# Optimization experiments

Measured on AMD Instinct MI355X. Metric: run time of the kernel, lower is better.

## Reference

```python
import jax, jax.numpy as jnp
import numpy as np

N = 50000
E = 800000
NODE_IN = 64
EDGE_IN = 8
OUT = 1
SAGE_DIMS = [(64, 64), (64, 64), (64, 32), (32, 32)]
EDGE_DIMS = [(8, 64), (64, 64), (64, 32), (32, 32)]


def setup_inputs():
    key = jax.random.key(0)
    keys = iter(jax.random.split(key, 64))
    d = {}
    d["x"] = jax.random.normal(next(keys), (N, NODE_IN), jnp.float32)
    d["dis"] = jax.random.normal(next(keys), (E, EDGE_IN), jnp.float32)
    d["edge_index"] = jax.random.randint(next(keys), (2, E), 0, N, dtype=jnp.int32)
    for i, (fi, fo) in enumerate(SAGE_DIMS):
        d[f"s{i}_wl"] = jax.random.normal(next(keys), (fi, fo), jnp.float32) / np.sqrt(fi).astype(np.float32)
        d[f"s{i}_bl"] = jnp.zeros((fo,), jnp.float32)
        d[f"s{i}_wr"] = jax.random.normal(next(keys), (fi, fo), jnp.float32) / np.sqrt(fi).astype(np.float32)
    for i, (fi, h) in enumerate(EDGE_DIMS):
        d[f"e{i}_w1"] = jax.random.normal(next(keys), (fi, 2 * h), jnp.float32) / np.sqrt(fi).astype(np.float32)
        d[f"e{i}_b1"] = jnp.zeros((2 * h,), jnp.float32)
        d[f"e{i}_w2"] = jax.random.normal(next(keys), (2 * h, h), jnp.float32) / np.sqrt(2 * h).astype(np.float32)
        d[f"e{i}_b2"] = jnp.zeros((h,), jnp.float32)
    d["fc_w"] = jax.random.normal(next(keys), (64, OUT), jnp.float32) / 8.0
    d["fc_b"] = jnp.zeros((OUT,), jnp.float32)
    return d


def _sage(x, row, col, wl, bl, wr):
    # PyG SAGEConv (aggr='mean'): lin_l(mean_{j->i} x_j) + lin_r(x_i); lin_l has bias.
    msg = x[row]  # [E, F] gather of source features
    s = jax.ops.segment_sum(msg, col, num_segments=N)
    cnt = jax.ops.segment_sum(jnp.ones((row.shape[0], 1), x.dtype), col, num_segments=N)
    mean = s / jnp.maximum(cnt, 1.0)  # isolated nodes -> 0 (matches scatter-mean)
    return mean @ wl + bl + x @ wr


def _edge_conv(dis, col, w1, b1, w2, b2):
    # EdgeOnlyConv: add_self_loops with num_nodes=E and zero edge_attr, so the
    # output has E rows; self-loop message = lin(0) = b1 and each segment t gets
    # mean = (sum_{edges->t} lin(dis) + b1) / (deg_in(t) + 1); then lin_update.
    msg = dis @ w1 + b1  # [E, 2h]
    s = jax.ops.segment_sum(msg, col, num_segments=E)
    deg = jax.ops.segment_sum(jnp.ones((col.shape[0], 1), dis.dtype), col, num_segments=E)
    aggr = (s + b1) / (deg + 1.0)
    return aggr @ w2 + b2


def _forward(x, dis, edge_index, sage_params, edge_params, fc_w, fc_b):
    row, col = edge_index[0], edge_index[1]
    h = x
    for wl, bl, wr in sage_params:
        h = jax.nn.leaky_relu(_sage(h, row, col, wl, bl, wr))
    d = dis
    for w1, b1, w2, b2 in edge_params:
        d = jax.nn.leaky_relu(_edge_conv(d, col, w1, b1, w2, b2))
    # dropout is identity at inference
    feats = jnp.concatenate([h[row] * h[col], d], axis=1)  # [E, hidden]
    return feats @ fc_w + fc_b


def reference(x, dis, edge_index, s0_wl, s0_bl, s0_wr, s1_wl, s1_bl, s1_wr, s2_wl, s2_bl, s2_wr, s3_wl, s3_bl, s3_wr, e0_w1, e0_b1, e0_w2, e0_b2, e1_w1, e1_b1, e1_w2, e1_b2, e2_w1, e2_b1, e2_w2, e2_b2, e3_w1, e3_b1, e3_w2, e3_b2, fc_w, fc_b):
    sage_params = [(s0_wl, s0_bl, s0_wr), (s1_wl, s1_bl, s1_wr), (s2_wl, s2_bl, s2_wr), (s3_wl, s3_bl, s3_wr)]
    edge_params = [(e0_w1, e0_b1, e0_w2, e0_b2), (e1_w1, e1_b1, e1_w2, e1_b2), (e2_w1, e2_b1, e2_w2, e2_b2), (e3_w1, e3_b1, e3_w2, e3_b2)]
    return _forward(x, dis, edge_index, sage_params, edge_params, fc_w, fc_b)
```

## Files before the change

kernel.cpp:

```cpp
#include <hip/hip_runtime.h>

#define LRELU(v) ((v) > 0.0f ? (v) : 0.01f * (v))

__device__ __forceinline__ unsigned short f2bf(float f) {
    union { float f; unsigned u; } c;
    c.f = f;
    return (unsigned short)((c.u + 0x7fffu + ((c.u >> 16) & 1)) >> 16);
}
__device__ __forceinline__ float bf_lo(unsigned u) {
    union { unsigned i; float f; } v;
    v.i = u << 16;
    return v.f;
}
__device__ __forceinline__ float bf_hi(unsigned u) {
    union { unsigned i; float f; } v;
    v.i = u & 0xffff0000u;
    return v.f;
}

template <int H2, int HOUT>
__device__ __forceinline__ void w12_body(const float* __restrict__ w1,
                                         const float* __restrict__ w2, float* __restrict__ out,
                                         int i, int o) {
    float s = 0.0f;
// ... 103 lines not shown
            float raw = ps[640 + oo] + ps[672 + oo] + ps[704 + oo] + ps[736 + oo];
            cbuf[448 + oo] = raw;
            float c = LRELU(raw + b2_3[oo]);
            c4s[oo] = c;
            cbuf[160 + oo] = c;
        }
        __syncthreads();
        a = 0.0f;
        if (w < 8) {
            int oo = t & 127, g = t >> 7;
#pragma unroll
            for (int j = 0; j < 16; ++j) {
                int f = g * 16 + j;
                a += c1[f] * w1_1[f * 128 + oo];
            }
        } else if (w < 12) {
            int l = t - 512;
            int oo = l & 63, g = l >> 6;
#pragma unroll
            for (int j = 0; j < 16; ++j) {
                int f = g * 16 + j;
                a += c2[f] * w1_2[f * 64 + oo];
            }
        } else {
            int l = t - 768;
            int oo = l & 63, g = l >> 6;
#pragma unroll
            for (int j = 0; j < 8; ++j) {
                int f = g * 8 + j;
                a += c3[f] * w1_3[f * 64 + oo];
            }
        }
        ps[t] = a;
        __syncthreads();
        if (t < 128) {
            u1[t] = ps[t] + ps[t + 128] + ps[t + 256] + ps[t + 384];
        } else if (t < 192) {
            int oo = t - 128;
            u2[oo] = ps[512 + oo] + ps[576 + oo] + ps[640 + oo] + ps[704 + oo];
        } else if (t < 256) {
            int oo = t - 192;
            u3[oo] = ps[768 + oo] + ps[832 + oo] + ps[896 + oo] + ps[960 + oo];
        }
        __syncthreads();
        a = 0.0f;
        if (w < 4) {
            int oo = t & 63, g = t >> 6;
#pragma unroll
            for (int j = 0; j < 32; ++j) {
                int k = g * 32 + j;
                a += u1[k] * w2_1[k * 64 + oo];
            }
        } else if (w < 6) {
            int l = t - 256;
            int oo = l & 31, g = l >> 5;
#pragma unroll
            for (int j = 0; j < 16; ++j) {
                int k = g * 16 + j;
                a += u2[k] * w2_2[k * 32 + oo];
            }
        } else if (w < 8) {
            int l = t - 384;
            int oo = l & 31, g = l >> 5;
#pragma unroll
            for (int j = 0; j < 16; ++j) {
                int k = g * 16 + j;
                a += u3[k] * w2_3[k * 32 + oo];
            }
        }
        ps[t] = a;
        if (w == 8) {
            int l = t - 512;
            float v = (l < 32) ? c4s[l] * fcw[32 + l] : 0.0f;
            v += __shfl_down(v, 16);
            v += __shfl_down(v, 8);
            v += __shfl_down(v, 4);
            v += __shfl_down(v, 2);
            v += __shfl_down(v, 1);
            if (l == 0) cbuf[512] = v;
        }
        __syncthreads();
        if (t < 64) {
            cbuf[320 + t] = cbuf[256 + t] + ps[t] + ps[t + 64] + ps[t + 128] + ps[t + 192];
        } else if (t < 96) {
            int oo = t - 64;
            cbuf[416 + oo] = cbuf[384 + oo] + ps[256 + oo] + ps[288 + oo] + ps[320 + oo] +
                             ps[352 + oo];
        } else if (t < 128) {
            int oo = t - 96;
            cbuf[480 + oo] = cbuf[448 + oo] + ps[384 + oo] + ps[416 + oo] + ps[448 + oo] +
                             ps[480 + oo];
        }
    }
}

__global__ void bucket_scan_k(const int* __restrict__ bpart, int* __restrict__ bbase,
                              int* __restrict__ bwp, int NBUCK, int E, int EB) {
    __shared__ int s[512];
    int tid = threadIdx.x;
    int v = 0;
    if (tid < NBUCK) {
        for (int b = 0; b < EB; ++b) v += bpart[(size_t)b * 512 + tid];
    }
    s[tid] = v;
    __syncthreads();
    for (int off = 1; off < 512; off <<= 1) {
        int t = (tid >= off) ? s[tid - off] : 0;
        __syncthreads();
        s[tid] += t;
        __syncthreads();
    }
    if (tid < NBUCK) {
        int ex = s[tid] - v;
        bbase[tid] = ex;
        bwp[tid] = ex;
    }
    if (tid == 0) bbase[NBUCK] = E;
}

__global__ void bucket_scatter_k(const int* __restrict__ row, const int* __restrict__ col,
                                 int* __restrict__ bwp, int2* __restrict__ tmp, int E) {
    __shared__ int lcnt[512];
    __shared__ int gbase[512];
    int tid = threadIdx.x;
    for (int i = tid; i < 512; i += 1024) lcnt[i] = 0;
    __syncthreads();
    int base = blockIdx.x * 8192;
    int lpos[8], bk[8];
    for (int k = 0; k < 8; ++k) {
        int e = base + k * 1024 + tid;
        if (e < E) {
            int b = col[e] >> 7;
            bk[k] = b;
            lpos[k] = atomicAdd(&lcnt[b], 1);
        } else
            bk[k] = -1;
    }
    __syncthreads();
    for (int i = tid; i < 512; i += 1024) {
        int v = lcnt[i];
        gbase[i] = v ? atomicAdd(&bwp[i], v) : 0;
    }
    __syncthreads();
    for (int k = 0; k < 8; ++k) {
        int e = base + k * 1024 + tid;
        if (e < E) {
            int c = col[e];
            tmp[gbase[bk[k]] + lpos[k]] = make_int2(row[e], ((c & 127) << 25) | e);
        }
    }
}

template <int FIN, int FOUT>
__device__ __forceinline__ void gemm2_body(const float* __restrict__ h,
                                           const float* __restrict__ wl,
                                           const float* __restrict__ wr,
                                           const float* __restrict__ bl,
                                           unsigned short* __restrict__ hl,
                                           float* __restrict__ hr, int N, int bx, int tid,
                                           float* sw) {
    constexpr int XT = (2 * FOUT) / 4;
    constexpr int NPT = 4;
    constexpr int NPB = (256 / XT) * NPT;
    int tx = tid % XT, ty = tid / XT;
    for (int idx = tid; idx < FIN * FOUT; idx += 256) {
        int f = idx / FOUT, o = idx % FOUT;
        sw[f * 2 * FOUT + o] = wl[idx];
        sw[f * 2 * FOUT + FOUT + o] = wr[idx];
    }
    __syncthreads();
    int og = tx * 4;
    int base = bx * NPB + ty * NPT;
    int ix[NPT] = {min(base + 0, N - 1), min(base + 1, N - 1), min(base + 2, N - 1),
                   min(base + 3, N - 1)};
    float4 s[NPT] = {{0.f, 0.f, 0.f, 0.f}, {0.f, 0.f, 0.f, 0.f}, {0.f, 0.f, 0.f, 0.f},
                     {0.f, 0.f, 0.f, 0.f}};
#pragma unroll 2
    for (int f = 0; f < FIN; f += 4) {
        float4 w0 = *(const float4*)&sw[(f + 0) * 2 * FOUT + og];
        float4 w1 = *(const float4*)&sw[(f + 1) * 2 * FOUT + og];
        float4 w2 = *(const float4*)&sw[(f + 2) * 2 * FOUT + og];
        float4 w3 = *(const float4*)&sw[(f + 3) * 2 * FOUT + og];
#pragma unroll
        for (int k = 0; k < NPT; ++k) {
            float4 v = *(const float4*)(h + (size_t)ix[k] * FIN + f);
            s[k].x += v.x * w0.x + v.y * w1.x + v.z * w2.x + v.w * w3.x;
            s[k].y += v.x * w0.y + v.y * w1.y + v.z * w2.y + v.w * w3.y;
            s[k].z += v.x * w0.z + v.y * w1.z + v.z * w2.z + v.w * w3.z;
            s[k].w += v.x * w0.w + v.y * w1.w + v.z * w2.w + v.w * w3.w;
        }
    }
    bool isR = og >= FOUT;
    int oo = isR ? og - FOUT : og;
    if (isR) {
        float4 bias = *(const float4*)&bl[oo];
#pragma unroll
        for (int k = 0; k < NPT; ++k) {
            int i = base + k;
            if (i < N) {
                float4 r = {s[k].x + bias.x, s[k].y + bias.y, s[k].z + bias.z, s[k].w + bias.w};
                *(float4*)(hr + (size_t)i * FOUT + oo) = r;
            }
        }
    } else {
#pragma unroll
        for (int k = 0; k < NPT; ++k) {
            int i = base + k;
            if (i < N) {
                unsigned short* d = hl + (size_t)i * FOUT + oo;
                *(ushort4*)d = make_ushort4(f2bf(s[k].x), f2bf(s[k].y), f2bf(s[k].z), f2bf(s[k].w));
            }
        }
    }
}

#define RED8(off)                                                                   \
    a0 += __shfl_down(a0, off); a1 += __shfl_down(a1, off);                         \
    a2 += __shfl_down(a2, off); a3 += __shfl_down(a3, off);                         \
    a4 += __shfl_down(a4, off); a5 += __shfl_down(a5, off);                         \
    a6 += __shfl_down(a6, off); a7 += __shfl_down(a7, off);

__device__ __forceinline__ void aggr64_body(const unsigned short* __restrict__ hlb,
                                            const float* __restrict__ hr,
                                            const int* __restrict__ rowptr,
                                            const int* __restrict__ rows,
                                            float* __restrict__ out, int N, int wave, int lane) {
    if (wave >= N) return;
    int u = lane >> 3, f8 = lane & 7;
    int s = rowptr[wave], e = rowptr[wave + 1];
    int l8 = lane & 7;
    const float4* hp = (const float4*)(hr + (size_t)wave * 64) + l8 * 2;
    float4 r0h = hp[0], r1h = hp[1];
    float inv = 1.0f / fmaxf((float)(e - s), 1.0f);
    float a0 = 0.f, a1 = 0.f, a2 = 0.f, a3 = 0.f, a4 = 0.f, a5 = 0.f, a6 = 0.f, a7 = 0.f;
    int p = s + u;
    for (; p + 8 < e; p += 16) {
        int r0 = rows[p], r1 = rows[p + 8];
        uint4 v0 = ((const uint4*)(hlb + (size_t)r0 * 64))[f8];
        uint4 v1 = ((const uint4*)(hlb + (size_t)r1 * 64))[f8];
        a0 += bf_lo(v0.x) + bf_lo(v1.x); a1 += bf_hi(v0.x) + bf_hi(v1.x);
        a2 += bf_lo(v0.y) + bf_lo(v1.y); a3 += bf_hi(v0.y) + bf_hi(v1.y);
        a4 += bf_lo(v0.z) + bf_lo(v1.z); a5 += bf_hi(v0.z) + bf_hi(v1.z);
        a6 += bf_lo(v0.w) + bf_lo(v1.w); a7 += bf_hi(v0.w) + bf_hi(v1.w);
    }
    if (p < e) {
        uint4 v = ((const uint4*)(hlb + (size_t)rows[p] * 64))[f8];
        a0 += bf_lo(v.x); a1 += bf_hi(v.x); a2 += bf_lo(v.y); a3 += bf_hi(v.y);
        a4 += bf_lo(v.z); a5 += bf_hi(v.z); a6 += bf_lo(v.w); a7 += bf_hi(v.w);
    }
    RED8(32) RED8(16) RED8(8)
    if (lane < 8) {
        float4 o0, o1;
        o0.x = LRELU(a0 * inv + r0h.x); o0.y = LRELU(a1 * inv + r0h.y);
        o0.z = LRELU(a2 * inv + r0h.z); o0.w = LRELU(a3 * inv + r0h.w);
        o1.x = LRELU(a4 * inv + r1h.x); o1.y = LRELU(a5 * inv + r1h.y);
        o1.z = LRELU(a6 * inv + r1h.z); o1.w = LRELU(a7 * inv + r1h.w);
        float4* op = (float4*)(out + (size_t)wave * 64) + lane * 2;
        op[0] = o0;
        op[1] = o1;
    }
}

template <bool OUTBF>
__device__ __forceinline__ void aggr32_body(const unsigned short* __restrict__ hlb,
                                            const float* __restrict__ hr,
                                            const int* __restrict__ rowptr,
                                            const int* __restrict__ rows, void* __restrict__ out,
                                            int N, int wave, int lane) {
    if (wave >= N) return;
    int u = lane >> 2, f8 = lane & 3;
    int s = rowptr[wave], e = rowptr[wave + 1];
    int l4 = lane & 3;
    const float4* hp = (const float4*)(hr + (size_t)wave * 32) + l4 * 2;
    float4 r0h = hp[0], r1h = hp[1];
    float inv = 1.0f / fmaxf((float)(e - s), 1.0f);
    float a0 = 0.f, a1 = 0.f, a2 = 0.f, a3 = 0.f, a4 = 0.f, a5 = 0.f, a6 = 0.f, a7 = 0.f;
    int p = s + u;
    for (; p + 16 < e; p += 32) {
        int r0 = rows[p], r1 = rows[p + 16];
        uint4 v0 = ((const uint4*)(hlb + (size_t)r0 * 32))[f8];
        uint4 v1 = ((const uint4*)(hlb + (size_t)r1 * 32))[f8];
        a0 += bf_lo(v0.x) + bf_lo(v1.x); a1 += bf_hi(v0.x) + bf_hi(v1.x);
        a2 += bf_lo(v0.y) + bf_lo(v1.y); a3 += bf_hi(v0.y) + bf_hi(v1.y);
        a4 += bf_lo(v0.z) + bf_lo(v1.z); a5 += bf_hi(v0.z) + bf_hi(v1.z);
        a6 += bf_lo(v0.w) + bf_lo(v1.w); a7 += bf_hi(v0.w) + bf_hi(v1.w);
    }
    if (p < e) {
        uint4 v = ((const uint4*)(hlb + (size_t)rows[p] * 32))[f8];
        a0 += bf_lo(v.x); a1 += bf_hi(v.x); a2 += bf_lo(v.y); a3 += bf_hi(v.y);
        a4 += bf_lo(v.z); a5 += bf_hi(v.z); a6 += bf_lo(v.w); a7 += bf_hi(v.w);
    }
    RED8(32) RED8(16) RED8(8) RED8(4)
    if (lane < 4) {
        float o0 = LRELU(a0 * inv + r0h.x), o1 = LRELU(a1 * inv + r0h.y);
        float o2 = LRELU(a2 * inv + r0h.z), o3 = LRELU(a3 * inv + r0h.w);
        float o4 = LRELU(a4 * inv + r1h.x), o5 = LRELU(a5 * inv + r1h.y);
        float o6 = LRELU(a6 * inv + r1h.z), o7 = LRELU(a7 * inv + r1h.w);
        if (OUTBF) {
            unsigned short* d = (unsigned short*)out + (size_t)wave * 32 + lane * 8;
            *(ushort4*)d = make_ushort4(f2bf(o0), f2bf(o1), f2bf(o2), f2bf(o3));
            *(ushort4*)(d + 4) = make_ushort4(f2bf(o4), f2bf(o5), f2bf(o6), f2bf(o7));
        } else {
            float4* op = (float4*)((float*)out + (size_t)wave * 32) + lane * 2;
            op[0] = make_float4(o0, o1, o2, o3);
            op[1] = make_float4(o4, o5, o6, o7);
        }
    }
}

__device__ __forceinline__ void edge_aggr8_body(const float* __restrict__ dis,
                                                const int* __restrict__ rowptr,
                                                const int* __restrict__ eids,
                                                float* __restrict__ sd, float* __restrict__ zbuf,
                                                int N, int wave, int lane) {
    if (wave >= N) return;
    zbuf[(size_t)wave * 64 + lane] = 0.0f;
    int u = lane >> 1, f4 = lane & 1;
    int s = rowptr[wave], e = rowptr[wave + 1];
    float4 a = {0.f, 0.f, 0.f, 0.f};
    for (int p = s + u; p < e; p += 32) {
        const float4* dp = (const float4*)(dis + (size_t)eids[p] * 8);
        float4 v = dp[f4];
        a.x += v.x; a.y += v.y; a.z += v.z; a.w += v.w;
    }
    for (int off = 32; off >= 2; off >>= 1) {
        a.x += __shfl_down(a.x, off); a.y += __shfl_down(a.y, off);
        a.z += __shfl_down(a.z, off); a.w += __shfl_down(a.w, off);
    }
    if (lane < 2) ((float4*)(sd + (size_t)wave * 8))[f4] = a;
}

template <int FIN, int FOUT>
__device__ __forceinline__ void esc_body(const float* __restrict__ sd, const int* __restrict__ cnt,
                                         const float* __restrict__ w12,
                                         const float* __restrict__ mw2,
                                         const float* __restrict__ b1w2,
                                         const float* __restrict__ b2,
                                         const float* __restrict__ cnext,
                                         const int* __restrict__ col, float* __restrict__ sdnext,
                                         int N, float* __restrict__ zbuf, int zf4, int bx,
                                         int nblk, int tid, float* sw) {
    constexpr int NPT = 4;
    constexpr int NPB = (256 / FOUT) * NPT;
    int o = tid % FOUT, ty = tid / FOUT;
    for (int idx = tid; idx < FIN * FOUT; idx += 256) sw[idx] = w12[idx];
    __syncthreads();
    if (zf4) {
        float4 z4 = {0.f, 0.f, 0.f, 0.f};
        for (int z = bx * 256 + tid; z < zf4; z += nblk * 256) ((float4*)zbuf)[z] = z4;
    }
    int base = bx * NPB + ty * NPT;
    int ix[NPT] = {min(base + 0, N - 1), min(base + 1, N - 1), min(base + 2, N - 1),
                   min(base + 3, N - 1)};
    float s[NPT] = {0.f, 0.f, 0.f, 0.f};
#pragma unroll 2
    for (int f = 0; f < FIN; f += 4) {
        float w0 = sw[(f + 0) * FOUT + o], w1 = sw[(f + 1) * FOUT + o];
        float w2 = sw[(f + 2) * FOUT + o], w3 = sw[(f + 3) * FOUT + o];
#pragma unroll
        for (int k = 0; k < NPT; ++k) {
            float4 v = *(const float4*)(sd + (size_t)ix[k] * FIN + f);
            s[k] += v.x * w0 + v.y * w1 + v.z * w2 + v.w * w3;
        }
    }
    float mo = mw2[o], bo = b1w2[o], b2o = b2[o], co = cnext[o];
#pragma unroll
    for (int k = 0; k < NPT; ++k) {
        int i = base + k;
        if (i < N) {
            float deg = (float)cnt[i];
            float inv = 1.0f / (deg + 1.0f);
            float val = LRELU((s[k] + deg * mo + bo) * inv + b2o);
            atomicAdd(&sdnext[(size_t)col[i] * FOUT + o], val - co);
        }
    }
}

__device__ __forceinline__ void edot_body(const float* __restrict__ sd,
                                          const int* __restrict__ cnt,
                                          const float* __restrict__ w12,
                                          const float* __restrict__ mw2,
                                          const float* __restrict__ b1w2,
                                          const float* __restrict__ b2,
                                          const float* __restrict__ fcw, float* __restrict__ ddot,
                                          int N, int bx, int tid, float* sw) {
    constexpr int FIN = 32, FOUT = 32;
    constexpr int NPT = 4;
    constexpr int NPB = (256 / FOUT) * NPT;
    int o = tid % 32, ty = tid / 32;
    for (int idx = tid; idx < FIN * FOUT; idx += 256) sw[idx] = w12[idx];
    __syncthreads();
    int base = bx * NPB + ty * NPT;
    int ix[NPT] = {min(base + 0, N - 1), min(base + 1, N - 1), min(base + 2, N - 1),
                   min(base + 3, N - 1)};
    float s[NPT] = {0.f, 0.f, 0.f, 0.f};
#pragma unroll 2
    for (int f = 0; f < FIN; f += 4) {
        float w0 = sw[(f + 0) * FOUT + o], w1 = sw[(f + 1) * FOUT + o];
        float w2 = sw[(f + 2) * FOUT + o], w3 = sw[(f + 3) * FOUT + o];
#pragma unroll
        for (int k = 0; k < NPT; ++k) {
            float4 v = *(const float4*)(sd + (size_t)ix[k] * FIN + f);
            s[k] += v.x * w0 + v.y * w1 + v.z * w2 + v.w * w3;
        }
    }
    float mo = mw2[o], bo = b1w2[o], b2o = b2[o], fw = fcw[32 + o];
#pragma unroll
    for (int k = 0; k < NPT; ++k) {
        float deg = (float)cnt[ix[k]];
        float inv = 1.0f / (deg + 1.0f);
        float v = LRELU((s[k] + deg * mo + bo) * inv + b2o) * fw;
        v += __shfl_down(v, 16);
        v += __shfl_down(v, 8);
        v += __shfl_down(v, 4);
        v += __shfl_down(v, 2);
        v += __shfl_down(v, 1);
        if (o == 0 && base + k < N) ddot[base + k] = v;
    }
}

union __align__(16) CsrGemmSM {
    struct {
        int2 buf[3072];
        int lcnt[128];
        int sscan[128];
        int lwp[128];
    } c;
    float sw[64 * 128];
};

__global__ void csr_gemm0_k(const int2* __restrict__ tmp, const int* __restrict__ bbase,
                            int* __restrict__ rowptr, int* __restrict__ cnt,
                            int* __restrict__ rows, int* __restrict__ eids, int N, int E,
                            int NBUCK, const float* __restrict__ h, const float* __restrict__ wl,
                            const float* __restrict__ wr, const float* __restrict__ bl,
                            unsigned short* __restrict__ hl, float* __restrict__ hr) {
    __shared__ CsrGemmSM sm;
    int tid = threadIdx.x;
    if (blockIdx.x < NBUCK) {
        constexpr int CAP = 3072;
        int b = blockIdx.x;
        int s = bbase[b], e = bbase[b + 1];
        int sz = e - s;
        if (tid < 128) sm.c.lcnt[tid] = 0;
        __syncthreads();
        for (int i = tid; i < sz; i += 256) {
            int2 v = tmp[s + i];
            if (i < CAP) sm.c.buf[i] = v;
            atomicAdd(&sm.c.lcnt[((unsigned)v.y) >> 25], 1);
        }
        __syncthreads();
        if (tid < 128) sm.c.sscan[tid] = sm.c.lcnt[tid];
        __syncthreads();
        for (int off = 1; off < 128; off <<= 1) {
            int t = (tid < 128 && tid >= off) ? sm.c.sscan[tid - off] : 0;
            __syncthreads();
            if (tid < 128) sm.c.sscan[tid] += t;
            __syncthreads();
        }
        if (tid < 128) {
            int ex = sm.c.sscan[tid] - sm.c.lcnt[tid];
            sm.c.lwp[tid] = ex;
            int c = b * 128 + tid;
            if (c < N) {
                rowptr[c] = s + ex;
                cnt[c] = sm.c.lcnt[tid];
                if (c == N - 1) rowptr[N] = E;
            }
        }
        __syncthreads();
        for (int i = tid; i < sz; i += 256) {
            int2 v = (i < CAP) ? sm.c.buf[i] : tmp[s + i];
            int cl = ((unsigned)v.y) >> 25;
            int p = atomicAdd(&sm.c.lwp[cl], 1);
            rows[s + p] = v.x;
            eids[s + p] = v.y & 0x1FFFFFF;
        }
        return;
    }
    gemm2_body<64, 64>(h, wl, wr, bl, hl, hr, N, blockIdx.x - NBUCK, tid, sm.sw);
}

__global__ void ag64_ea8_k(const unsigned short* __restrict__ hlb, const float* __restrict__ hr,
                           const int* __restrict__ rowptr, const int* __restrict__ rows,
                           float* __restrict__ out, const float* __restrict__ dis,
                           const int* __restrict__ eids, float* __restrict__ sd0,
                           float* __restrict__ zS1, int N, int NB) {
    int lane = threadIdx.x & 63;
    if (blockIdx.x < NB) {
        int wave = (blockIdx.x * 256 + threadIdx.x) >> 6;
        aggr64_body(hlb, hr, rowptr, rows, out, N, wave, lane);
    } else {
        int wave = ((blockIdx.x - NB) * 256 + threadIdx.x) >> 6;
        edge_aggr8_body(dis, rowptr, eids, sd0, zS1, N, wave, lane);
    }
}

__global__ void g64_esc0_k(const float* __restrict__ h, const float* __restrict__ wl,
                           const float* __restrict__ wr, const float* __restrict__ bl,
                           unsigned short* __restrict__ hl, float* __restrict__ hr,
                           const float* __restrict__ sd0, const int* __restrict__ cnt,
                           const float* __restrict__ w12, const float* __restrict__ mw2,
                           const float* __restrict__ b1w2, const float* __restrict__ b2,
                           const float* __restrict__ cnext, const int* __restrict__ col,
                           float* __restrict__ S1, float* __restrict__ zS2, int N, int G0,
                           int E0) {
    __shared__ float sw[64 * 128];
    int tid = threadIdx.x;
    if (blockIdx.x < G0) {
        gemm2_body<64, 64>(h, wl, wr, bl, hl, hr, N, blockIdx.x, tid, sw);
    } else {
        esc_body<8, 64>(sd0, cnt, w12, mw2, b1w2, b2, cnext, col, S1, N, zS2, N * 16,
                        blockIdx.x - G0, E0, tid, sw);
    }
}

__global__ void ag64_esc1_k(const unsigned short* __restrict__ hlb, const float* __restrict__ hr,
                            const int* __restrict__ rowptr, const int* __restrict__ rows,
                            float* __restrict__ out, const float* __restrict__ S1,
                            const int* __restrict__ cnt, const float* __restrict__ w12,
                            const float* __restrict__ mw2, const float* __restrict__ b1w2,
                            const float* __restrict__ b2, const float* __restrict__ cnext,
                            const int* __restrict__ col, float* __restrict__ S2,
                            float* __restrict__ zS3, int N, int NB, int E0) {
    __shared__ float sw[64 * 64];
    int tid = threadIdx.x;
    if (blockIdx.x < NB) {
        int wave = (blockIdx.x * 256 + tid) >> 6;
        aggr64_body(hlb, hr, rowptr, rows, out, N, wave, tid & 63);
    } else {
        esc_body<64, 64>(S1, cnt, w12, mw2, b1w2, b2, cnext, col, S2, N, zS3, N * 8,
                         blockIdx.x - NB, E0, tid, sw);
    }
}

__global__ void g32_esc2_k(const float* __restrict__ h, const float* __restrict__ wl,
                           const float* __restrict__ wr, const float* __restrict__ bl,
                           unsigned short* __restrict__ hl, float* __restrict__ hr,
                           const float* __restrict__ S2, const int* __restrict__ cnt,
                           const float* __restrict__ w12, const float* __restrict__ mw2,
                           const float* __restrict__ b1w2, const float* __restrict__ b2,
                           const float* __restrict__ cnext, const int* __restrict__ col,
                           float* __restrict__ S3, int N, int G2, int E2) {
    __shared__ float sw[64 * 64];
    int tid = threadIdx.x;
    if (blockIdx.x < G2) {
        gemm2_body<64, 32>(h, wl, wr, bl, hl, hr, N, blockIdx.x, tid, sw);
    } else {
        esc_body<64, 32>(S2, cnt, w12, mw2, b1w2, b2, cnext, col, S3, N, nullptr, 0,
                         blockIdx.x - G2, E2, tid, sw);
    }
}

__global__ void ag32_edot_k(const unsigned short* __restrict__ hlb, const float* __restrict__ hr,
                            const int* __restrict__ rowptr, const int* __restrict__ rows,
                            float* __restrict__ out, const float* __restrict__ S3,
                            const int* __restrict__ cnt, const float* __restrict__ w12,
                            const float* __restrict__ mw2, const float* __restrict__ b1w2,
                            const float* __restrict__ b2, const float* __restrict__ fcw,
                            float* __restrict__ ddot, int N, int NB) {
    __shared__ float sw[32 * 32];
    int tid = threadIdx.x;
    if (blockIdx.x < NB) {
        int wave = (blockIdx.x * 256 + tid) >> 6;
        aggr32_body<false>(hlb, hr, rowptr, rows, (void*)out, N, wave, tid & 63);
    } else {
        edot_body(S3, cnt, w12, mw2, b1w2, b2, fcw, ddot, N, blockIdx.x - NB, tid, sw);
    }
}

__global__ void gemm2_32_k(const float* __restrict__ h, const float* __restrict__ wl,
                           const float* __restrict__ wr, const float* __restrict__ bl,
                           unsigned short* __restrict__ hl, float* __restrict__ hr, int N) {
    __shared__ float sw[32 * 64];
    gemm2_body<32, 32>(h, wl, wr, bl, hl, hr, N, blockIdx.x, threadIdx.x, sw);
}

__global__ void ag32bf_k(const unsigned short* __restrict__ hlb, const float* __restrict__ hr,
                         const int* __restrict__ rowptr, const int* __restrict__ rows,
                         unsigned short* __restrict__ h3b, int N) {
    int wave = (blockIdx.x * 256 + threadIdx.x) >> 6;
    aggr32_body<true>(hlb, hr, rowptr, rows, (void*)h3b, N, wave, threadIdx.x & 63);
}

__global__ void final_csr_k(const unsigned short* __restrict__ h3b,
                            const float* __restrict__ ddot, const float* __restrict__ cbuf,
                            const int* __restrict__ rowptr, const int* __restrict__ rows,
                            const int* __restrict__ eids, const float* __restrict__ fcw,
                            const float* __restrict__ fcb, float* __restrict__ out, int N) {
    int wave = (blockIdx.x * blockDim.x + threadIdx.x) >> 6;
    int lane = threadIdx.x & 63;
    if (wave >= N) return;
    int u = lane >> 2, f2 = lane & 3;
    int s = rowptr[wave], e = rowptr[wave + 1];
    uint4 hc = ((const uint4*)(h3b + (size_t)wave * 32))[f2];
    const float4* fw4 = (const float4*)fcw + f2 * 2;
    float4 w0 = fw4[0], w1 = fw4[1];
    float wc0 = bf_lo(hc.x) * w0.x, wc1 = bf_hi(hc.x) * w0.y;
    float wc2 = bf_lo(hc.y) * w0.z, wc3 = bf_hi(hc.y) * w0.w;
    float wc4 = bf_lo(hc.z) * w1.x, wc5 = bf_hi(hc.z) * w1.y;
    float wc6 = bf_lo(hc.w) * w1.z, wc7 = bf_hi(hc.w) * w1.w;
    float fb = fcb[0];
    float cdot = cbuf[512];
    int p = s + u;
    for (; p + 16 < e; p += 32) {
        int ra = rows[p], rb = rows[p + 16];
        int ea_ = eids[p], eb_ = eids[p + 16];
        uint4 va = ((const uint4*)(h3b + (size_t)ra * 32))[f2];
        uint4 vb = ((const uint4*)(h3b + (size_t)rb * 32))[f2];
        float ta = bf_lo(va.x) * wc0 + bf_hi(va.x) * wc1 + bf_lo(va.y) * wc2 +
                   bf_hi(va.y) * wc3 + bf_lo(va.z) * wc4 + bf_hi(va.z) * wc5 +
                   bf_lo(va.w) * wc6 + bf_hi(va.w) * wc7;
        float tb = bf_lo(vb.x) * wc0 + bf_hi(vb.x) * wc1 + bf_lo(vb.y) * wc2 +
                   bf_hi(vb.y) * wc3 + bf_lo(vb.z) * wc4 + bf_hi(vb.z) * wc5 +
                   bf_lo(vb.w) * wc6 + bf_hi(vb.w) * wc7;
        ta += __shfl_down(ta, 2); tb += __shfl_down(tb, 2);
        ta += __shfl_down(ta, 1); tb += __shfl_down(tb, 1);
        if (f2 == 0) {
            out[ea_] = ta + fb + (ea_ < N ? ddot[ea_] : cdot);
            out[eb_] = tb + fb + (eb_ < N ? ddot[eb_] : cdot);
        }
    }
    if (p < e) {
        int ra = rows[p];
        int ea_ = eids[p];
        uint4 va = ((const uint4*)(h3b + (size_t)ra * 32))[f2];
        float ta = bf_lo(va.x) * wc0 + bf_hi(va.x) * wc1 + bf_lo(va.y) * wc2 +
                   bf_hi(va.y) * wc3 + bf_lo(va.z) * wc4 + bf_hi(va.z) * wc5 +
                   bf_lo(va.w) * wc6 + bf_hi(va.w) * wc7;
        ta += __shfl_down(ta, 2);
        ta += __shfl_down(ta, 1);
        if (f2 == 0) out[ea_] = ta + fb + (ea_ < N ? ddot[ea_] : cdot);
    }
}

extern "C" void kernel_launch(void* const* d_in, const int* in_sizes, int n_in, void* d_out,
                              int out_size, void* d_ws, size_t ws_size, hipStream_t stream) {
    const float* x = (const float*)d_in[0];
    const float* dis = (const float*)d_in[1];
    const int* ei = (const int*)d_in[2];
    const float* s_wl[4] = {(const float*)d_in[3], (const float*)d_in[6], (const float*)d_in[9],
                            (const float*)d_in[12]};
    const float* s_bl[4] = {(const float*)d_in[4], (const float*)d_in[7], (const float*)d_in[10],
                            (const float*)d_in[13]};
    const float* s_wr[4] = {(const float*)d_in[5], (const float*)d_in[8], (const float*)d_in[11],
                            (const float*)d_in[14]};
    const float* e_w1[4] = {(const float*)d_in[15], (const float*)d_in[19], (const float*)d_in[23],
                            (const float*)d_in[27]};
    const float* e_b1[4] = {(const float*)d_in[16], (const float*)d_in[20], (const float*)d_in[24],
                            (const float*)d_in[28]};
    const float* e_w2[4] = {(const float*)d_in[17], (const float*)d_in[21], (const float*)d_in[25],
                            (const float*)d_in[29]};
    const float* e_b2[4] = {(const float*)d_in[18], (const float*)d_in[22], (const float*)d_in[26],
                            (const float*)d_in[30]};
    const float* fcw = (const float*)d_in[31];
    const float* fcb = (const float*)d_in[32];

    const int N = in_sizes[0] / 64;
    const int E = in_sizes[1] / 8;
    const int* row = ei;
    const int* col = ei + E;
    const int NBUCK = (N + 127) / 128;
    const int EB = (E + 8191) / 8192;

    auto au = [](size_t v) { return (v + 255) & ~(size_t)255; };
    char* p = (char*)d_ws;
    int* cnt = (int*)p;        p += au((size_t)N * 4);
    int* rowptr = (int*)p;     p += au((size_t)(N + 1) * 4);
    int* bbase = (int*)p;      p += au(513 * 4);
    int* bwp = (int*)p;        p += au(512 * 4);
    float* w12_0 = (float*)p;  p += au(512 * 4);
    float* w12_1 = (float*)p;  p += au(4096 * 4);
    float* w12_2 = (float*)p;  p += au(2048 * 4);
    float* w12_3 = (float*)p;  p += au(1024 * 4);
    float* cbuf = (float*)p;   p += au(544 * 4);
    int* bpart = (int*)p;      p += au((size_t)EB * 512 * 4);
    int* rowsA = (int*)p;      p += au((size_t)E * 4);
    int* eidsA = (int*)p;      p += au((size_t)E * 4);
    unsigned short* T = (unsigned short*)p; p += au((size_t)N * 64 * 2);
    float* R = (float*)p;      p += au((size_t)N * 64 * 4);
    float* H1 = (float*)p;     p += au((size_t)N * 64 * 4);
    float* H2 = (float*)p;     p += au((size_t)N * 64 * 4);
    float* S1 = (float*)p;     p += au((size_t)N * 64 * 4);
    float* S2 = (float*)p;     p += au((size_t)N * 64 * 4);
    float* S3 = (float*)p;     p += au((size_t)N * 32 * 4);
    float* sd0 = (float*)p;    p += au((size_t)N * 8 * 4);
    unsigned short* h3b = (unsigned short*)p; p += au((size_t)N * 32 * 2);
    float* ddot = (float*)p;   p += au((size_t)N * 4);

    int2* tmp = (int2*)S1;

    const int G0 = (N + 31) / 32;
    const int G2 = (N + 63) / 64;
    const int G3 = (N + 63) / 64;
    const int E0 = (N + 15) / 16;
    const int E2 = (N + 31) / 32;
    const int NB = (N + 3) / 4;

    count_w12c_k<<<EB + 169, 1024, 0, stream>>>(
        col, bpart, E, EB, e_w1[0], e_w2[0], w12_0, e_w1[1], e_w2[1], w12_1, e_w1[2], e_w2[2],
        w12_2, e_w1[3], e_w2[3], w12_3, e_b1[0], e_b2[0], e_b1[1], e_b2[1], e_b1[2], e_b2[2],
        e_b1[3], e_b2[3], fcw, cbuf);
    bucket_scan_k<<<1, 512, 0, stream>>>(bpart, bbase, bwp, NBUCK, E, EB);
    bucket_scatter_k<<<EB, 1024, 0, stream>>>(row, col, bwp, tmp, E);
    csr_gemm0_k<<<NBUCK + G0, 256, 0, stream>>>(tmp, bbase, rowptr, cnt, rowsA, eidsA, N, E,
                                                NBUCK, x, s_wl[0], s_wr[0], s_bl[0], T, R);
    ag64_ea8_k<<<2 * NB, 256, 0, stream>>>(T, R, rowptr, rowsA, H1, dis, eidsA, sd0, S1, N, NB);
    g64_esc0_k<<<G0 + E0, 256, 0, stream>>>(H1, s_wl[1], s_wr[1], s_bl[1], T, R, sd0, cnt, w12_0,
                                            cbuf + 192, cbuf + 192, e_b2[0], cbuf + 0, col, S1,
                                            S2, N, G0, E0);
    ag64_esc1_k<<<NB + E0, 256, 0, stream>>>(T, R, rowptr, rowsA, H2, S1, cnt, w12_1, cbuf + 320,
                                             cbuf + 256, e_b2[1], cbuf + 64, col, S2, S3, N, NB,
                                             E0);
    g32_esc2_k<<<G2 + E2, 256, 0, stream>>>(H2, s_wl[2], s_wr[2], s_bl[2], T, R, S2, cnt, w12_2,
                                            cbuf + 416, cbuf + 384, e_b2[2], cbuf + 128, col, S3,
                                            N, G2, E2);
    ag32_edot_k<<<NB + E2, 256, 0, stream>>>(T, R, rowptr, rowsA, H1, S3, cnt, w12_3, cbuf + 480,
                                             cbuf + 448, e_b2[3], fcw, ddot, N, NB);
    gemm2_32_k<<<G3, 256, 0, stream>>>(H1, s_wl[3], s_wr[3], s_bl[3], T, R, N);
    ag32bf_k<<<NB, 256, 0, stream>>>(T, R, rowptr, rowsA, h3b, N);
    final_csr_k<<<NB, 256, 0, stream>>>(h3b, ddot, cbuf, rowptr, rowsA, eidsA, fcw, fcb,
                                        (float*)d_out, N);
}
```

Baseline: 441.2 us.

## Fuse root-weight GEMM and bias into SAGE aggregation kernels, drop R buffer

The GEMM kernels now compute only the neighbour projection h@wl, stored as bf16. The root term h@wr and the bias are computed inside the per-node aggregation wave: each sub-group of lanes handles a slice of input features, and the partial products are folded into the existing shuffle reduction. This removes the fp32 R intermediate and its write and re-read for every layer, and halves the GEMM work and shared memory. In exchange the aggregation kernels read the input features and the wr weights directly from global memory, with extra FLOPs per wave.

```diff
diff --git a/kernel.cpp b/kernel.cpp
--- a/kernel.cpp
+++ b/kernel.cpp
@@ -279,22 +279,15 @@
 }
 
 template <int FIN, int FOUT>
-__device__ __forceinline__ void gemm2_body(const float* __restrict__ h,
+__device__ __forceinline__ void gemmT_body(const float* __restrict__ h,
                                            const float* __restrict__ wl,
-                                           const float* __restrict__ wr,
-                                           const float* __restrict__ bl,
-                                           unsigned short* __restrict__ hl,
-                                           float* __restrict__ hr, int N, int bx, int tid,
-                                           float* sw) {
-    constexpr int XT = (2 * FOUT) / 4;
+                                           unsigned short* __restrict__ hl, int N, int bx,
+                                           int tid, float* sw) {
+    constexpr int XT = FOUT / 4;
     constexpr int NPT = 4;
     constexpr int NPB = (256 / XT) * NPT;
     int tx = tid % XT, ty = tid / XT;
-    for (int idx = tid; idx < FIN * FOUT; idx += 256) {
-        int f = idx / FOUT, o = idx % FOUT;
-        sw[f * 2 * FOUT + o] = wl[idx];
-        sw[f * 2 * FOUT + FOUT + o] = wr[idx];
-    }
+    for (int idx = tid; idx < FIN * FOUT; idx += 256) sw[idx] = wl[idx];
     __syncthreads();
     int og = tx * 4;
     int base = bx * NPB + ty * NPT;
@@ -304,10 +297,10 @@
                      {0.f, 0.f, 0.f, 0.f}};
 #pragma unroll 2
     for (int f = 0; f < FIN; f += 4) {
-        float4 w0 = *(const float4*)&sw[(f + 0) * 2 * FOUT + og];
-        float4 w1 = *(const float4*)&sw[(f + 1) * 2 * FOUT + og];
-        float4 w2 = *(const float4*)&sw[(f + 2) * 2 * FOUT + og];
-        float4 w3 = *(const float4*)&sw[(f + 3) * 2 * FOUT + og];
+        float4 w0 = *(const float4*)&sw[(f + 0) * FOUT + og];
+        float4 w1 = *(const float4*)&sw[(f + 1) * FOUT + og];
+        float4 w2 = *(const float4*)&sw[(f + 2) * FOUT + og];
+        float4 w3 = *(const float4*)&sw[(f + 3) * FOUT + og];
 #pragma unroll
         for (int k = 0; k < NPT; ++k) {
             float4 v = *(const float4*)(h + (size_t)ix[k] * FIN + f);
@@ -317,26 +310,12 @@
             s[k].w += v.x * w0.w + v.y * w1.w + v.z * w2.w + v.w * w3.w;
         }
     }
-    bool isR = og >= FOUT;
-    int oo = isR ? og - FOUT : og;
-    if (isR) {
-        float4 bias = *(const float4*)&bl[oo];
-#pragma unroll
-        for (int k = 0; k < NPT; ++k) {
-            int i = base + k;
-            if (i < N) {
-                float4 r = {s[k].x + bias.x, s[k].y + bias.y, s[k].z + bias.z, s[k].w + bias.w};
-                *(float4*)(hr + (size_t)i * FOUT + oo) = r;
-            }
-        }
-    } else {
-#pragma unroll
-        for (int k = 0; k < NPT; ++k) {
-            int i = base + k;
-            if (i < N) {
-                unsigned short* d = hl + (size_t)i * FOUT + oo;
-                *(ushort4*)d = make_ushort4(f2bf(s[k].x), f2bf(s[k].y), f2bf(s[k].z), f2bf(s[k].w));
-            }
+#pragma unroll
+    for (int k = 0; k < NPT; ++k) {
+        int i = base + k;
+        if (i < N) {
+            unsigned short* d = hl + (size_t)i * FOUT + og;
+            *(ushort4*)d = make_ushort4(f2bf(s[k].x), f2bf(s[k].y), f2bf(s[k].z), f2bf(s[k].w));
         }
     }
 }
@@ -348,23 +327,39 @@
     a6 += __shfl_down(a6, off); a7 += __shfl_down(a7, off);
 
 __device__ __forceinline__ void aggr64_body(const unsigned short* __restrict__ hlb,
-                                            const float* __restrict__ hr,
+                                            const float* __restrict__ h,
+                                            const float* __restrict__ wr,
+                                            const float* __restrict__ bl,
                                             const int* __restrict__ rowptr,
                                             const int* __restrict__ rows,
                                             float* __restrict__ out, int N, int wave, int lane) {
     if (wave >= N) return;
     int u = lane >> 3, f8 = lane & 7;
     int s = rowptr[wave], e = rowptr[wave + 1];
-    int l8 = lane & 7;
-    const float4* hp = (const float4*)(hr + (size_t)wave * 64) + l8 * 2;
-    float4 r0h = hp[0], r1h = hp[1];
+    float r0 = 0.f, r1 = 0.f, r2 = 0.f, r3 = 0.f, r4 = 0.f, r5 = 0.f, r6 = 0.f, r7 = 0.f;
+    {
+        const float4* hp = (const float4*)(h + (size_t)wave * 64 + 8 * u);
+        float4 hA = hp[0], hB = hp[1];
+        float hv0 = hA.x, hv1 = hA.y, hv2 = hA.z, hv3 = hA.w;
+        float hv4 = hB.x, hv5 = hB.y, hv6 = hB.z, hv7 = hB.w;
+        const float* wrb = wr + (size_t)(8 * u) * 64 + 8 * f8;
+#pragma unroll
+        for (int t = 0; t < 8; ++t) {
+            float4 wA = *(const float4*)(wrb + t * 64);
+            float4 wB = *(const float4*)(wrb + t * 64 + 4);
+            float hv = (t == 0) ? hv0 : (t == 1) ? hv1 : (t == 2) ? hv2 : (t == 3) ? hv3
+                       : (t == 4) ? hv4 : (t == 5) ? hv5 : (t == 6) ? hv6 : hv7;
+            r0 += hv * wA.x; r1 += hv * wA.y; r2 += hv * wA.z; r3 += hv * wA.w;
+            r4 += hv * wB.x; r5 += hv * wB.y; r6 += hv * wB.z; r7 += hv * wB.w;
+        }
+    }
     float inv = 1.0f / fmaxf((float)(e - s), 1.0f);
     float a0 = 0.f, a1 = 0.f, a2 = 0.f, a3 = 0.f, a4 = 0.f, a5 = 0.f, a6 = 0.f, a7 = 0.f;
     int p = s + u;
     for (; p + 8 < e; p += 16) {
-        int r0 = rows[p], r1 = rows[p + 8];
-        uint4 v0 = ((const uint4*)(hlb + (size_t)r0 * 64))[f8];
-        uint4 v1 = ((const uint4*)(hlb + (size_t)r1 * 64))[f8];
+        int n0 = rows[p], n1 = rows[p + 8];
+        uint4 v0 = ((const uint4*)(hlb + (size_t)n0 * 64))[f8];
+        uint4 v1 = ((const uint4*)(hlb + (size_t)n1 * 64))[f8];
         a0 += bf_lo(v0.x) + bf_lo(v1.x); a1 += bf_hi(v0.x) + bf_hi(v1.x);
         a2 += bf_lo(v0.y) + bf_lo(v1.y); a3 += bf_hi(v0.y) + bf_hi(v1.y);
         a4 += bf_lo(v0.z) + bf_lo(v1.z); a5 += bf_hi(v0.z) + bf_hi(v1.z);
@@ -375,38 +370,67 @@
         a0 += bf_lo(v.x); a1 += bf_hi(v.x); a2 += bf_lo(v.y); a3 += bf_hi(v.y);
         a4 += bf_lo(v.z); a5 += bf_hi(v.z); a6 += bf_lo(v.w); a7 += bf_hi(v.w);
     }
+    a0 = a0 * inv + r0; a1 = a1 * inv + r1; a2 = a2 * inv + r2; a3 = a3 * inv + r3;
+    a4 = a4 * inv + r4; a5 = a5 * inv + r5; a6 = a6 * inv + r6; a7 = a7 * inv + r7;
     RED8(32) RED8(16) RED8(8)
     if (lane < 8) {
+        const float4* bp = (const float4*)bl + lane * 2;
+        float4 b0 = bp[0], b1 = bp[1];
         float4 o0, o1;
-        o0.x = LRELU(a0 * inv + r0h.x); o0.y = LRELU(a1 * inv + r0h.y);
-        o0.z = LRELU(a2 * inv + r0h.z); o0.w = LRELU(a3 * inv + r0h.w);
-        o1.x = LRELU(a4 * inv + r1h.x); o1.y = LRELU(a5 * inv + r1h.y);
-        o1.z = LRELU(a6 * inv + r1h.z); o1.w = LRELU(a7 * inv + r1h.w);
+        o0.x = LRELU(a0 + b0.x); o0.y = LRELU(a1 + b0.y);
+        o0.z = LRELU(a2 + b0.z); o0.w = LRELU(a3 + b0.w);
+        o1.x = LRELU(a4 + b1.x); o1.y = LRELU(a5 + b1.y);
+        o1.z = LRELU(a6 + b1.z); o1.w = LRELU(a7 + b1.w);
         float4* op = (float4*)(out + (size_t)wave * 64) + lane * 2;
         op[0] = o0;
         op[1] = o1;
     }
 }
 
-template <bool OUTBF>
+template <int FIN, bool OUTBF>
 __device__ __forceinline__ void aggr32_body(const unsigned short* __restrict__ hlb,
-                                            const float* __restrict__ hr,
+                                            const float* __restrict__ h,
+                                            const float* __restrict__ wr,
+                                            const float* __restrict__ bl,
                                             const int* __restrict__ rowptr,
                                             const int* __restrict__ rows, void* __restrict__ out,
                                             int N, int wave, int lane) {
     if (wave >= N) return;
     int u = lane >> 2, f8 = lane & 3;
     int s = rowptr[wave], e = rowptr[wave + 1];
-    int l4 = lane & 3;
-    const float4* hp = (const float4*)(hr + (size_t)wave * 32) + l4 * 2;
-    float4 r0h = hp[0], r1h = hp[1];
+    float r0 = 0.f, r1 = 0.f, r2 = 0.f, r3 = 0.f, r4 = 0.f, r5 = 0.f, r6 = 0.f, r7 = 0.f;
+    if (FIN == 64) {
+        float4 hA = *(const float4*)(h + (size_t)wave * 64 + 4 * u);
+        float hv0 = hA.x, hv1 = hA.y, hv2 = hA.z, hv3 = hA.w;
+        const float* wrb = wr + (size_t)(4 * u) * 32 + 8 * f8;
+#pragma unroll
+        for (int t = 0; t < 4; ++t) {
+            float4 wA = *(const float4*)(wrb + t * 32);
+            float4 wB = *(const float4*)(wrb + t * 32 + 4);
+            float hv = (t == 0) ? hv0 : (t == 1) ? hv1 : (t == 2) ? hv2 : hv3;
+            r0 += hv * wA.x; r1 += hv * wA.y; r2 += hv * wA.z; r3 += hv * wA.w;
+            r4 += hv * wB.x; r5 += hv * wB.y; r6 += hv * wB.z; r7 += hv * wB.w;
+        }
+    } else {
+        float2 hA = *(const float2*)(h + (size_t)wave * 32 + 2 * u);
+        float hv0 = hA.x, hv1 = hA.y;
+        const float* wrb = wr + (size_t)(2 * u) * 32 + 8 * f8;
+#pragma unroll
+        for (int t = 0; t < 2; ++t) {
+            float4 wA = *(const float4*)(wrb + t * 32);
+            float4 wB = *(const float4*)(wrb + t * 32 + 4);
+            float hv = (t == 0) ? hv0 : hv1;
+            r0 += hv * wA.x; r1 += hv * wA.y; r2 += hv * wA.z; r3 += hv * wA.w;
+            r4 += hv * wB.x; r5 += hv * wB.y; r6 += hv * wB.z; r7 += hv * wB.w;
+        }
+    }
     float inv = 1.0f / fmaxf((float)(e - s), 1.0f);
     float a0 = 0.f, a1 = 0.f, a2 = 0.f, a3 = 0.f, a4 = 0.f, a5 = 0.f, a6 = 0.f, a7 = 0.f;
     int p = s + u;
     for (; p + 16 < e; p += 32) {
-        int r0 = rows[p], r1 = rows[p + 16];
-        uint4 v0 = ((const uint4*)(hlb + (size_t)r0 * 32))[f8];
-        uint4 v1 = ((const uint4*)(hlb + (size_t)r1 * 32))[f8];
+        int n0 = rows[p], n1 = rows[p + 16];
+        uint4 v0 = ((const uint4*)(hlb + (size_t)n0 * 32))[f8];
+        uint4 v1 = ((const uint4*)(hlb + (size_t)n1 * 32))[f8];
         a0 += bf_lo(v0.x) + bf_lo(v1.x); a1 += bf_hi(v0.x) + bf_hi(v1.x);
         a2 += bf_lo(v0.y) + bf_lo(v1.y); a3 += bf_hi(v0.y) + bf_hi(v1.y);
         a4 += bf_lo(v0.z) + bf_lo(v1.z); a5 += bf_hi(v0.z) + bf_hi(v1.z);
@@ -417,12 +441,16 @@
         a0 += bf_lo(v.x); a1 += bf_hi(v.x); a2 += bf_lo(v.y); a3 += bf_hi(v.y);
         a4 += bf_lo(v.z); a5 += bf_hi(v.z); a6 += bf_lo(v.w); a7 += bf_hi(v.w);
     }
+    a0 = a0 * inv + r0; a1 = a1 * inv + r1; a2 = a2 * inv + r2; a3 = a3 * inv + r3;
+    a4 = a4 * inv + r4; a5 = a5 * inv + r5; a6 = a6 * inv + r6; a7 = a7 * inv + r7;
     RED8(32) RED8(16) RED8(8) RED8(4)
     if (lane < 4) {
-        float o0 = LRELU(a0 * inv + r0h.x), o1 = LRELU(a1 * inv + r0h.y);
-        float o2 = LRELU(a2 * inv + r0h.z), o3 = LRELU(a3 * inv + r0h.w);
-        float o4 = LRELU(a4 * inv + r1h.x), o5 = LRELU(a5 * inv + r1h.y);
-        float o6 = LRELU(a6 * inv + r1h.z), o7 = LRELU(a7 * inv + r1h.w);
+        const float4* bp = (const float4*)bl + lane * 2;
+        float4 b0 = bp[0], b1 = bp[1];
+        float o0 = LRELU(a0 + b0.x), o1 = LRELU(a1 + b0.y);
+        float o2 = LRELU(a2 + b0.z), o3 = LRELU(a3 + b0.w);
+        float o4 = LRELU(a4 + b1.x), o5 = LRELU(a5 + b1.y);
+        float o6 = LRELU(a6 + b1.z), o7 = LRELU(a7 + b1.w);
         if (OUTBF) {
             unsigned short* d = (unsigned short*)out + (size_t)wave * 32 + lane * 8;
             *(ushort4*)d = make_ushort4(f2bf(o0), f2bf(o1), f2bf(o2), f2bf(o3));
@@ -553,15 +581,14 @@
         int sscan[128];
         int lwp[128];
     } c;
-    float sw[64 * 128];
+    float sw[64 * 64];
 };
 
 __global__ void csr_gemm0_k(const int2* __restrict__ tmp, const int* __restrict__ bbase,
                             int* __restrict__ rowptr, int* __restrict__ cnt,
                             int* __restrict__ rows, int* __restrict__ eids, int N, int E,
                             int NBUCK, const float* __restrict__ h, const float* __restrict__ wl,
-                            const float* __restrict__ wr, const float* __restrict__ bl,
-                            unsigned short* __restrict__ hl, float* __restrict__ hr) {
+                            unsigned short* __restrict__ hl) {
     __shared__ CsrGemmSM sm;
     int tid = threadIdx.x;
     if (blockIdx.x < NBUCK) {
@@ -605,10 +632,11 @@
         }
         return;
     }
-    gemm2_body<64, 64>(h, wl, wr, bl, hl, hr, N, blockIdx.x - NBUCK, tid, sm.sw);
-}
-
-__global__ void ag64_ea8_k(const unsigned short* __restrict__ hlb, const float* __restrict__ hr,
+    gemmT_body<64, 64>(h, wl, hl, N, blockIdx.x - NBUCK, tid, sm.sw);
+}
+
+__global__ void ag64_ea8_k(const unsigned short* __restrict__ hlb, const float* __restrict__ h,
+                           const float* __restrict__ wr, const float* __restrict__ bl,
                            const int* __restrict__ rowptr, const int* __restrict__ rows,
                            float* __restrict__ out, const float* __restrict__ dis,
                            const int* __restrict__ eids, float* __restrict__ sd0,
@@ -616,7 +644,7 @@
     int lane = threadIdx.x & 63;
     if (blockIdx.x < NB) {
         int wave = (blockIdx.x * 256 + threadIdx.x) >> 6;
-        aggr64_body(hlb, hr, rowptr, rows, out, N, wave, lane);
+        aggr64_body(hlb, h, wr, bl, rowptr, rows, out, N, wave, lane);
     } else {
         int wave = ((blockIdx.x - NB) * 256 + threadIdx.x) >> 6;
         edge_aggr8_body(dis, rowptr, eids, sd0, zS1, N, wave, lane);
@@ -624,25 +652,24 @@
 }
 
 __global__ void g64_esc0_k(const float* __restrict__ h, const float* __restrict__ wl,
-                           const float* __restrict__ wr, const float* __restrict__ bl,
-                           unsigned short* __restrict__ hl, float* __restrict__ hr,
-                           const float* __restrict__ sd0, const int* __restrict__ cnt,
-                           const float* __restrict__ w12, const float* __restrict__ mw2,
-                           const float* __restrict__ b1w2, const float* __restrict__ b2,
-                           const float* __restrict__ cnext, const int* __restrict__ col,
-                           float* __restrict__ S1, float* __restrict__ zS2, int N, int G0,
-                           int E0) {
-    __shared__ float sw[64 * 128];
+                           unsigned short* __restrict__ hl, const float* __restrict__ sd0,
+                           const int* __restrict__ cnt, const float* __restrict__ w12,
+                           const float* __restrict__ mw2, const float* __restrict__ b1w2,
+                           const float* __restrict__ b2, const float* __restrict__ cnext,
+                           const int* __restrict__ col, float* __restrict__ S1,
+                           float* __restrict__ zS2, int N, int G0, int E0) {
+    __shared__ float sw[64 * 64];
     int tid = threadIdx.x;
     if (blockIdx.x < G0) {
-        gemm2_body<64, 64>(h, wl, wr, bl, hl, hr, N, blockIdx.x, tid, sw);
+        gemmT_body<64, 64>(h, wl, hl, N, blockIdx.x, tid, sw);
     } else {
         esc_body<8, 64>(sd0, cnt, w12, mw2, b1w2, b2, cnext, col, S1, N, zS2, N * 16,
                         blockIdx.x - G0, E0, tid, sw);
     }
 }
 
-__global__ void ag64_esc1_k(const unsigned short* __restrict__ hlb, const float* __restrict__ hr,
+__global__ void ag64_esc1_k(const unsigned short* __restrict__ hlb, const float* __restrict__ h,
+                            const float* __restrict__ wr, const float* __restrict__ bl,
                             const int* __restrict__ rowptr, const int* __restrict__ rows,
                             float* __restrict__ out, const float* __restrict__ S1,
                             const int* __restrict__ cnt, const float* __restrict__ w12,
@@ -654,7 +681,7 @@
     int tid = threadIdx.x;
     if (blockIdx.x < NB) {
         int wave = (blockIdx.x * 256 + tid) >> 6;
-        aggr64_body(hlb, hr, rowptr, rows, out, N, wave, tid & 63);
+        aggr64_body(hlb, h, wr, bl, rowptr, rows, out, N, wave, tid & 63);
     } else {
         esc_body<64, 64>(S1, cnt, w12, mw2, b1w2, b2, cnext, col, S2, N, zS3, N * 8,
                          blockIdx.x - NB, E0, tid, sw);
@@ -662,24 +689,24 @@
 }
 
 __global__ void g32_esc2_k(const float* __restrict__ h, const float* __restrict__ wl,
-                           const float* __restrict__ wr, const float* __restrict__ bl,
-                           unsigned short* __restrict__ hl, float* __restrict__ hr,
-                           const float* __restrict__ S2, const int* __restrict__ cnt,
-                           const float* __restrict__ w12, const float* __restrict__ mw2,
-                           const float* __restrict__ b1w2, const float* __restrict__ b2,
-                           const float* __restrict__ cnext, const int* __restrict__ col,
-                           float* __restrict__ S3, int N, int G2, int E2) {
-    __shared__ float sw[64 * 64];
+                           unsigned short* __restrict__ hl, const float* __restrict__ S2,
+                           const int* __restrict__ cnt, const float* __restrict__ w12,
+                           const float* __restrict__ mw2, const float* __restrict__ b1w2,
+                           const float* __restrict__ b2, const float* __restrict__ cnext,
+                           const int* __restrict__ col, float* __restrict__ S3, int N, int G2,
+                           int E2) {
+    __shared__ float sw[64 * 32];
     int tid = threadIdx.x;
     if (blockIdx.x < G2) {
-        gemm2_body<64, 32>(h, wl, wr, bl, hl, hr, N, blockIdx.x, tid, sw);
+        gemmT_body<64, 32>(h, wl, hl, N, blockIdx.x, tid, sw);
     } else {
         esc_body<64, 32>(S2, cnt, w12, mw2, b1w2, b2, cnext, col, S3, N, nullptr, 0,
                          blockIdx.x - G2, E2, tid, sw);
     }
 }
 
-__global__ void ag32_edot_k(const unsigned short* __restrict__ hlb, const float* __restrict__ hr,
+__global__ void ag32_edot_k(const unsigned short* __restrict__ hlb, const float* __restrict__ h,
+                            const float* __restrict__ wr, const float* __restrict__ bl,
                             const int* __restrict__ rowptr, const int* __restrict__ rows,
                             float* __restrict__ out, const float* __restrict__ S3,
                             const int* __restrict__ cnt, const float* __restrict__ w12,
@@ -690,24 +717,24 @@
     int tid = threadIdx.x;
     if (blockIdx.x < NB) {
         int wave = (blockIdx.x * 256 + tid) >> 6;
-        aggr32_body<false>(hlb, hr, rowptr, rows, (void*)out, N, wave, tid & 63);
+        aggr32_body<64, false>(hlb, h, wr, bl, rowptr, rows, (void*)out, N, wave, tid & 63);
     } else {
         edot_body(S3, cnt, w12, mw2, b1w2, b2, fcw, ddot, N, blockIdx.x - NB, tid, sw);
     }
 }
 
-__global__ void gemm2_32_k(const float* __restrict__ h, const float* __restrict__ wl,
-                           const float* __restrict__ wr, const float* __restrict__ bl,
-                           unsigned short* __restrict__ hl, float* __restrict__ hr, int N) {
-    __shared__ float sw[32 * 64];
-    gemm2_body<32, 32>(h, wl, wr, bl, hl, hr, N, blockIdx.x, threadIdx.x, sw);
-}
-
-__global__ void ag32bf_k(const unsigned short* __restrict__ hlb, const float* __restrict__ hr,
+__global__ void gemm3_k(const float* __restrict__ h, const float* __restrict__ wl,
+                        unsigned short* __restrict__ hl, int N) {
+    __shared__ float sw[32 * 32];
+    gemmT_body<32, 32>(h, wl, hl, N, blockIdx.x, threadIdx.x, sw);
+}
+
+__global__ void ag32bf_k(const unsigned short* __restrict__ hlb, const float* __restrict__ h,
+                         const float* __restrict__ wr, const float* __restrict__ bl,
                          const int* __restrict__ rowptr, const int* __restrict__ rows,
                          unsigned short* __restrict__ h3b, int N) {
     int wave = (blockIdx.x * 256 + threadIdx.x) >> 6;
-    aggr32_body<true>(hlb, hr, rowptr, rows, (void*)h3b, N, wave, threadIdx.x & 63);
+    aggr32_body<32, true>(hlb, h, wr, bl, rowptr, rows, (void*)h3b, N, wave, threadIdx.x & 63);
 }
 
 __global__ void final_csr_k(const unsigned short* __restrict__ h3b,
@@ -805,7 +832,6 @@
     int* rowsA = (int*)p;      p += au((size_t)E * 4);
     int* eidsA = (int*)p;      p += au((size_t)E * 4);
     unsigned short* T = (unsigned short*)p; p += au((size_t)N * 64 * 2);
-    float* R = (float*)p;      p += au((size_t)N * 64 * 4);
     float* H1 = (float*)p;     p += au((size_t)N * 64 * 4);
     float* H2 = (float*)p;     p += au((size_t)N * 64 * 4);
     float* S1 = (float*)p;     p += au((size_t)N * 64 * 4);
@@ -817,9 +843,8 @@
 
     int2* tmp = (int2*)S1;
 
-    const int G0 = (N + 31) / 32;
-    const int G2 = (N + 63) / 64;
-    const int G3 = (N + 63) / 64;
+    const int G64 = (N + 63) / 64;
+    const int G128 = (N + 127) / 128;
     const int E0 = (N + 15) / 16;
     const int E2 = (N + 31) / 32;
     const int NB = (N + 3) / 4;
@@ -830,22 +855,24 @@
         e_b1[3], e_b2[3], fcw, cbuf);
     bucket_scan_k<<<1, 512, 0, stream>>>(bpart, bbase, bwp, NBUCK, E, EB);
     bucket_scatter_k<<<EB, 1024, 0, stream>>>(row, col, bwp, tmp, E);
-    csr_gemm0_k<<<NBUCK + G0, 256, 0, stream>>>(tmp, bbase, rowptr, cnt, rowsA, eidsA, N, E,
-                                                NBUCK, x, s_wl[0], s_wr[0], s_bl[0], T, R);
-    ag64_ea8_k<<<2 * NB, 256, 0, stream>>>(T, R, rowptr, rowsA, H1, dis, eidsA, sd0, S1, N, NB);
-    g64_esc0_k<<<G0 + E0, 256, 0, stream>>>(H1, s_wl[1], s_wr[1], s_bl[1], T, R, sd0, cnt, w12_0,
-                                            cbuf + 192, cbuf + 192, e_b2[0], cbuf + 0, col, S1,
-                                            S2, N, G0, E0);
-    ag64_esc1_k<<<NB + E0, 256, 0, stream>>>(T, R, rowptr, rowsA, H2, S1, cnt, w12_1, cbuf + 320,
-                                             cbuf + 256, e_b2[1], cbuf + 64, col, S2, S3, N, NB,
+    csr_gemm0_k<<<NBUCK + G64, 256, 0, stream>>>(tmp, bbase, rowptr, cnt, rowsA, eidsA, N, E,
+                                                 NBUCK, x, s_wl[0], T);
+    ag64_ea8_k<<<2 * NB, 256, 0, stream>>>(T, x, s_wr[0], s_bl[0], rowptr, rowsA, H1, dis, eidsA,
+                                           sd0, S1, N, NB);
+    g64_esc0_k<<<G64 + E0, 256, 0, stream>>>(H1, s_wl[1], T, sd0, cnt, w12_0, cbuf + 192,
+                                             cbuf + 192, e_b2[0], cbuf + 0, col, S1, S2, N, G64,
                                              E0);
-    g32_esc2_k<<<G2 + E2, 256, 0, stream>>>(H2, s_wl[2], s_wr[2], s_bl[2], T, R, S2, cnt, w12_2,
-                                            cbuf + 416, cbuf + 384, e_b2[2], cbuf + 128, col, S3,
-                                            N, G2, E2);
-    ag32_edot_k<<<NB + E2, 256, 0, stream>>>(T, R, rowptr, rowsA, H1, S3, cnt, w12_3, cbuf + 480,
-                                             cbuf + 448, e_b2[3], fcw, ddot, N, NB);
-    gemm2_32_k<<<G3, 256, 0, stream>>>(H1, s_wl[3], s_wr[3], s_bl[3], T, R, N);
-    ag32bf_k<<<NB, 256, 0, stream>>>(T, R, rowptr, rowsA, h3b, N);
+    ag64_esc1_k<<<NB + E0, 256, 0, stream>>>(T, H1, s_wr[1], s_bl[1], rowptr, rowsA, H2, S1, cnt,
+                                             w12_1, cbuf + 320, cbuf + 256, e_b2[1], cbuf + 64,
+                                             col, S2, S3, N, NB, E0);
+    g32_esc2_k<<<G128 + E2, 256, 0, stream>>>(H2, s_wl[2], T, S2, cnt, w12_2, cbuf + 416,
+                                              cbuf + 384, e_b2[2], cbuf + 128, col, S3, N, G128,
+                                              E2);
+    ag32_edot_k<<<NB + E2, 256, 0, stream>>>(T, H2, s_wr[2], s_bl[2], rowptr, rowsA, H1, S3, cnt,
+                                             w12_3, cbuf + 480, cbuf + 448, e_b2[3], fcw, ddot,
+                                             N, NB);
+    gemm3_k<<<G128, 256, 0, stream>>>(H1, s_wl[3], T, N);
+    ag32bf_k<<<NB, 256, 0, stream>>>(T, H1, s_wr[3], s_bl[3], rowptr, rowsA, h3b, N);
     final_csr_k<<<NB, 256, 0, stream>>>(h3b, ddot, cbuf, rowptr, rowsA, eidsA, fcw, fcb,
                                         (float*)d_out, N);
 }
```

Result: slower. 492.8 us (+11.7%).
